# Kernel optimization log

Measured on AMD Instinct MI355X. Metric: run time of the kernel, lower is better.

## Reference

```python
import jax, jax.numpy as jnp
import numpy as np

N, F, H, C = 50000, 128, 256, 40
E = 800000
L, J = 3, 2
TOT = 7  # sum_{i<L} J**i


def setup_inputs() -> dict:
    key = jax.random.key(0)
    ks = jax.random.split(key, 16)
    def rn(k, shape, scale):
        return jax.random.normal(k, shape, jnp.float32) * scale
    w = lambda k, shape: rn(k, shape, 1.0 / np.sqrt(shape[0]).astype(np.float32))
    return {
        "x": rn(ks[0], (N, F), 1.0),
        "feature": rn(ks[1], (TOT, N, F), 1.0),
        "src": jax.random.randint(ks[2], (E,), 0, N),
        "dst": jax.random.randint(ks[3], (E,), 0, N),
        "conv_W0": w(ks[4], (F, H)),       "conv_b0": jnp.zeros((H,), jnp.float32),
        "conv_W1": w(ks[5], (2 * H, H)),   "conv_b1": jnp.zeros((H,), jnp.float32),
        "conv_W2": w(ks[6], (2 * H, H)),   "conv_b2": jnp.zeros((H,), jnp.float32),
        "lin_W0": w(ks[7], (F, H)),        "lin_b0": jnp.zeros((H,), jnp.float32),
        "lin_W1": w(ks[8], (2 * F, H)),    "lin_b1": jnp.zeros((H,), jnp.float32),
        "lin_W2": w(ks[9], (4 * F, H)),    "lin_b2": jnp.zeros((H,), jnp.float32),
        "order_weights": rn(ks[10], (J,), 1.0 / np.sqrt(J).astype(np.float32)),
        "cls_W": w(ks[11], (2 * H, C)),    "cls_b": jnp.zeros((C,), jnp.float32),
    }


def reference(x, feature, src, dst,
              conv_W0, conv_b0, conv_W1, conv_b1, conv_W2, conv_b2,
              lin_W0, lin_b0, lin_W1, lin_b1, lin_W2, lin_b2,
              order_weights, cls_W, cls_b):
    # GCN normalization with self-loops (A-hat = D^-1/2 (A+I) D^-1/2)
    loop = jnp.arange(N, dtype=src.dtype)
    src_sl = jnp.concatenate([src, loop])   # [E+N]
    dst_sl = jnp.concatenate([dst, loop])
    deg = jax.ops.segment_sum(jnp.ones_like(dst_sl, jnp.float32), dst_sl, num_segments=N)
    dinv = jax.lax.rsqrt(deg)  # deg >= 1 thanks to self loops
    norm = dinv[src_sl] * dinv[dst_sl]      # [E+N]

    def gcn(h, W, b):
        m = h @ W                            # transform first (smaller gather)
        agg = jax.ops.segment_sum(m[src_sl] * norm[:, None], dst_sl, num_segments=N)
        return agg + b

    conv_W = [conv_W0, conv_W1, conv_W2]
    conv_b = [conv_b0, conv_b1, conv_b2]
    lin_W = [lin_W0, lin_W1, lin_W2]
    lin_b = [lin_b0, lin_b1, lin_b2]

    comb = x
    begin = 0
    for i in range(L):
        convx = jax.nn.relu(gcn(comb, conv_W[i], conv_b[i]))  # [N, H]
        count = J ** i
        lf = feature[begin:begin + count]                      # [count, N, F]
        if i > 0:
            ow = jnp.tile(order_weights, J ** (i - 1)).reshape(-1, 1, 1)
            lf = ow * lf
        lf = jnp.moveaxis(lf, 0, 1).reshape(N, count * F)      # [N, count*F]
        lin_sct = jax.nn.relu(lf @ lin_W[i] + lin_b[i])        # [N, H]
        comb = jnp.concatenate([lin_sct, convx], axis=-1)      # [N, 2H]
        begin += count
    logits = gcn(comb, cls_W, cls_b)                           # [N, C]
    return jax.nn.log_softmax(logits, axis=-1), logits
```

## Files before the change

### kernel.cpp

```cpp
#include <hip/hip_runtime.h>

#define DEVI __device__ __forceinline__

namespace {

constexpr int Nn = 50000;
constexpr int Ne = 800000;
constexpr int Fd = 128;
constexpr int Hd = 256;
constexpr int Cd = 40;
constexpr int NB = (Nn + 255) / 256;

typedef __attribute__((ext_vector_type(8))) short s16x8;
typedef __attribute__((ext_vector_type(8))) unsigned short u16x8;
typedef __attribute__((ext_vector_type(4))) float f32x4;

DEVI unsigned short f2bf(float f) {
  unsigned int u = __builtin_bit_cast(unsigned int, f);
  u += 0x7fffu + ((u >> 16) & 1u);
  return (unsigned short)(u >> 16);
}
DEVI float bf2f(unsigned short s) {
  return __builtin_bit_cast(float, ((unsigned int)s) << 16);
}

DEVI void gld_lds16(const void* gptr, void* lds_base) {
  const unsigned m0v =
      (unsigned)__builtin_amdgcn_readfirstlane((unsigned)(uintptr_t)lds_base);
  asm volatile("s_mov_b32 m0, %0\n\t"
               "global_load_lds_dwordx4 %1, off"
               :: "s"(m0v), "v"(gptr) : "memory");
}

DEVI void wait_vm0_lgkm0() {
  asm volatile("s_waitcnt vmcnt(0) lgkmcnt(0)" ::: "memory");
}

DEVI void wt_one(const float* __restrict__ W, unsigned short* __restrict__ Wt,
                 int idx, int K, int H, const float* __restrict__ ow) {
  int c = idx / K, k = idx - c * K;
  int kt = k >> 6, c16 = (k >> 3) & 7, j = k & 7;
  int ksrc = (kt << 6) | ((c16 ^ (c & 7)) << 3) | j;
  float v = (c < H) ? W[(size_t)ksrc * H + c] : 0.0f;
  if (ow) v *= ow[(ksrc >> 7) & 1];
  Wt[idx] = f2bf(v);
}

constexpr int WTO0 = 0;
constexpr int WTO1 = WTO0 + 256 * 128;
constexpr int WTO2 = WTO1 + 256 * 512;
constexpr int WTO3 = WTO2 + 256 * 512;
constexpr int WTO4 = WTO3 + 256 * 128;
constexpr int WTO5 = WTO4 + 256 * 256;
constexpr int WTO6 = WTO5 + 256 * 512;
constexpr int WTO7 = WTO6 + 64 * 512;
constexpr int PREPTOT = WTO7 + Nn;

__global__ __launch_bounds__(256) void k_prep(
    const float* W0, const float* W1, const float* W2, const float* W3,
    const float* W4, const float* W5, const float* W6, const float* ow,
    unsigned short* T0, unsigned short* T1, unsigned short* T2, unsigned short* T3,
    unsigned short* T4, unsigned short* T5, unsigned short* T6, int* cnt) {
  int idx = blockIdx.x * 256 + threadIdx.x;
  if (idx >= PREPTOT) return;
  if (idx < WTO1)      wt_one(W0, T0, idx - WTO0, 128, 256, nullptr);
  else if (idx < WTO2) wt_one(W1, T1, idx - WTO1, 512, 256, nullptr);
  else if (idx < WTO3) wt_one(W2, T2, idx - WTO2, 512, 256, nullptr);
  else if (idx < WTO4) wt_one(W3, T3, idx - WTO3, 128, 256, nullptr);
  else if (idx < WTO5) wt_one(W4, T4, idx - WTO4, 256, 256, ow);
  else if (idx < WTO6) wt_one(W5, T5, idx - WTO5, 512, 256, ow);
  else if (idx < WTO7) wt_one(W6, T6, idx - WTO6, 512, 40, nullptr);
  else cnt[idx - WTO7] = 0;
}

__global__ void k_count(const int* __restrict__ dst, int* __restrict__ cnt) {
  int e = blockIdx.x * 256 + threadIdx.x;
  if (e < Ne) atomicAdd(&cnt[dst[e]], 1);
}

__global__ __launch_bounds__(256) void k_partial(const int* __restrict__ cnt,
                                                 int* __restrict__ partial) {
  __shared__ int red[256];
  const int t = threadIdx.x;
  const int i = blockIdx.x * 256 + t;
  red[t] = (i < Nn) ? cnt[i] + 1 : 0;
  __syncthreads();
#pragma unroll
  for (int off = 128; off; off >>= 1) {
    if (t < off) red[t] += red[t + off];
    __syncthreads();
  }
  if (t == 0) partial[blockIdx.x] = red[0];
}

__global__ __launch_bounds__(256) void k_scan_small(const int* __restrict__ partial,
                                                    int* __restrict__ poffs,
                                                    int* __restrict__ rowptr) {
  __shared__ int s[256];
  const int t = threadIdx.x;
  const int v = (t < NB) ? partial[t] : 0;
  s[t] = v;
  __syncthreads();
#pragma unroll
  for (int off = 1; off < 256; off <<= 1) {
    int add = (t >= off) ? s[t - off] : 0;
    __syncthreads();
    s[t] += add;
    __syncthreads();
  }
  if (t < NB) poffs[t] = s[t] - v;
  if (t == NB - 1) rowptr[Nn] = s[t];
}

__global__ __launch_bounds__(256) void k_rowptr(const int* __restrict__ cnt,
                                                const int* __restrict__ poffs,
                                                int* __restrict__ rowptr,
                                                int* __restrict__ cursor,
                                                float* __restrict__ dinv) {
  __shared__ int s[256];
  const int t = threadIdx.x;
  const int i = blockIdx.x * 256 + t;
  const int c = (i < Nn) ? cnt[i] + 1 : 0;
  s[t] = c;
  __syncthreads();
#pragma unroll
  for (int off = 1; off < 256; off <<= 1) {
    int add = (t >= off) ? s[t - off] : 0;
    __syncthreads();
    s[t] += add;
    __syncthreads();
  }
  if (i < Nn) {
    const int excl = s[t] - c + poffs[blockIdx.x];
    rowptr[i] = excl;
    cursor[i] = excl;
    dinv[i] = rsqrtf((float)c);
  }
}

__global__ void k_fill(const int* __restrict__ src, const int* __restrict__ dst,
                       const float* __restrict__ dinv, int* __restrict__ cursor,
                       int* __restrict__ csrs, float* __restrict__ csrn) {
  int e = blockIdx.x * 256 + threadIdx.x;
  if (e < Ne) {
    int s = src[e], d = dst[e];
    int pos = atomicAdd(&cursor[d], 1);
    csrs[pos] = s;
    csrn[pos] = dinv[s] * dinv[d];
  } else if (e < Ne + Nn) {
    int d = e - Ne;
    int pos = atomicAdd(&cursor[d], 1);
    csrs[pos] = d;
    float v = dinv[d];
    csrn[pos] = v * v;
  }
}

struct GRole {
  const float* A;
  const unsigned short* Wt;
  const float* bias;
  unsigned short* C;
  int K;
  int ldc;
  int relu;
};

__global__ __launch_bounds__(256) void k_gemm4(GRole R0, GRole R1, GRole R2, GRole R3) {
  const GRole R = (blockIdx.y == 0) ? R0 : (blockIdx.y == 1) ? R1
                  : (blockIdx.y == 2) ? R2 : R3;
  __shared__ char smem[49152];
  short* lA0 = (short*)smem;
  short* lA1 = (short*)(smem + 8192);
  short* lB  = (short*)(smem + 16384);
  const int tid = threadIdx.x;
  const int lane = tid & 63;
  const int wid = tid >> 6;
  const int wc = wid;
  const int row0 = blockIdx.x * 64;
  const size_t NnF = (size_t)Nn * Fd;

  f32x4 acc[4][4];
#pragma unroll
  for (int i = 0; i < 4; ++i)
#pragma unroll
    for (int j = 0; j < 4; ++j) acc[i][j] = (f32x4)0.0f;

  auto issueA = [&](int kt, f32x4 (&A4)[2][2]) {
    const int k0 = kt * 64;
    const int c = k0 >> 7;
    const int f0 = k0 & 127;
#pragma unroll
    for (int i = 0; i < 2; ++i) {
      const int v = tid * 2 + i;
      const int row = v >> 3, c16 = v & 7;
      const int grow = row0 + row;
      const bool rv = grow < Nn;
      const float* p = R.A + (size_t)c * NnF + (size_t)grow * Fd + f0 + c16 * 8;
      A4[i][0] = rv ? *(const f32x4*)p : (f32x4)0.0f;
      A4[i][1] = rv ? *(const f32x4*)(p + 4) : (f32x4)0.0f;
    }
  };
  auto writeA = [&](f32x4 (&A4)[2][2], short* lAb) {
#pragma unroll
    for (int i = 0; i < 2; ++i) {
      const int v = tid * 2 + i;
      const int row = v >> 3, c16 = v & 7;
      s16x8 val;
#pragma unroll
      for (int q = 0; q < 4; ++q) val[q] = (short)f2bf(A4[i][0][q]);
#pragma unroll
      for (int q = 0; q < 4; ++q) val[4 + q] = (short)f2bf(A4[i][1][q]);
      int byte = row * 128 + c16 * 16;
      byte ^= (row & 7) << 4;
      *(s16x8*)((char*)lAb + byte) = val;
    }
  };
  auto stageB = [&](int kt) {
    const int k0 = kt * 64;
#pragma unroll
    for (int i = 0; i < 8; ++i) {
      const int iss = wid * 8 + i;
      const int col = iss * 8 + (lane >> 3);
      gld_lds16(R.Wt + (size_t)col * R.K + k0 + (lane & 7) * 8, lB + iss * 512);
    }
  };
  auto readB = [&](s16x8 (&bv)[2][4]) {
#pragma unroll
    for (int kk = 0; kk < 2; ++kk)
#pragma unroll
      for (int ni = 0; ni < 4; ++ni) {
        int c = wc * 64 + ni * 16 + (lane & 15);
        int byte = c * 128 + kk * 64 + (lane >> 4) * 16;
        byte ^= (c & 7) << 4;
        bv[kk][ni] = *(const s16x8*)((const char*)lB + byte);
      }
  };
  auto mfma = [&](const short* lAb, s16x8 (&bv)[2][4]) {
#pragma unroll
    for (int kk = 0; kk < 2; ++kk) {
      s16x8 af[4];
#pragma unroll
      for (int mi = 0; mi < 4; ++mi) {
        int r = mi * 16 + (lane & 15);
        int byte = r * 128 + kk * 64 + (lane >> 4) * 16;
        byte ^= (r & 7) << 4;
        af[mi] = *(const s16x8*)((const char*)lAb + byte);
      }
#pragma unroll
      for (int mi = 0; mi < 4; ++mi)
#pragma unroll
        for (int ni = 0; ni < 4; ++ni)
          acc[mi][ni] = __builtin_amdgcn_mfma_f32_16x16x32_bf16(af[mi], bv[kk][ni], acc[mi][ni], 0, 0, 0);
    }
  };

  const int nkt = R.K >> 6;
  f32x4 Areg[2][2];
  issueA(0, Areg);
  stageB(0);
  writeA(Areg, lA0);
  wait_vm0_lgkm0();
  __builtin_amdgcn_s_barrier();
  for (int kt = 0; kt < nkt; ++kt) {
    short* curA = (kt & 1) ? lA1 : lA0;
    short* nxtA = (kt & 1) ? lA0 : lA1;
    s16x8 bv[2][4];
    readB(bv);
    asm volatile("s_waitcnt lgkmcnt(0)" ::: "memory");
    if (kt + 1 < nkt) { issueA(kt + 1, Areg); stageB(kt + 1); }
    mfma(curA, bv);
    if (kt + 1 < nkt) writeA(Areg, nxtA);
    wait_vm0_lgkm0();
    __builtin_amdgcn_s_barrier();
  }

  short* lC = (short*)smem;
#pragma unroll
  for (int ni = 0; ni < 4; ++ni) {
    const int col = wc * 64 + ni * 16 + (lane & 15);
    const float bvl = R.bias ? R.bias[col] : 0.0f;
#pragma unroll
    for (int mi = 0; mi < 4; ++mi) {
      const int rb = mi * 16 + ((lane >> 4) << 2);
#pragma unroll
      for (int q = 0; q < 4; ++q) {
        float vv = acc[mi][ni][q] + bvl;
        if (R.relu) vv = fmaxf(vv, 0.0f);
        lC[(rb + q) * 256 + col] = f2bf(vv);
      }
    }
  }
  __syncthreads();
#pragma unroll
  for (int p = 0; p < 8; ++p) {
    const int idx = (p * 256 + tid) * 8;
    const int row = idx >> 8;
    const int col = idx & 255;
    const int r = row0 + row;
    if (r < Nn)
      *(u16x8*)(R.C + (size_t)r * R.ldc + col) = *(const u16x8*)(lC + idx);
  }
}

__global__ __launch_bounds__(256) void k_gemmC(
    const unsigned short* __restrict__ A, int lda, int K,
    const unsigned short* __restrict__ Wt, unsigned short* __restrict__ C,
    int ldc) {
  __shared__ char smem[49152];
  short* lA0 = (short*)smem;
  short* lA1 = (short*)(smem + 8192);
  short* lB  = (short*)(smem + 16384);
  const int tid = threadIdx.x;
  const int lane = tid & 63;
  const int wid = tid >> 6;
  const int wc = wid;
  const int row0 = blockIdx.x * 64;
  const int c16a = (lane & 7) ^ ((lane >> 3) & 7);

  f32x4 acc[4][4];
#pragma unroll
  for (int i = 0; i < 4; ++i)
#pragma unroll
    for (int j = 0; j < 4; ++j) acc[i][j] = (f32x4)0.0f;

  auto stageA = [&](int kt, short* lAb) {
    const int k0 = kt * 64;
#pragma unroll
    for (int i = 0; i < 2; ++i) {
      const int iss = wid * 2 + i;
      const int row = row0 + iss * 8 + (lane >> 3);
      gld_lds16(A + (size_t)row * lda + k0 + c16a * 8, lAb + iss * 512);
    }
  };
  auto stageB = [&](int kt) {
    const int k0 = kt * 64;
#pragma unroll
    for (int i = 0; i < 8; ++i) {
      const int iss = wid * 8 + i;
      const int col = iss * 8 + (lane >> 3);
      gld_lds16(Wt + (size_t)col * K + k0 + (lane & 7) * 8, lB + iss * 512);
    }
  };
  auto readB = [&](s16x8 (&bv)[2][4]) {
#pragma unroll
    for (int kk = 0; kk < 2; ++kk)
#pragma unroll
      for (int ni = 0; ni < 4; ++ni) {
        int c = wc * 64 + ni * 16 + (lane & 15);
        int byte = c * 128 + kk * 64 + (lane >> 4) * 16;
        byte ^= (c & 7) << 4;
        bv[kk][ni] = *(const s16x8*)((const char*)lB + byte);
      }
  };
  auto mfma = [&](const short* lAb, s16x8 (&bv)[2][4]) {
#pragma unroll
    for (int kk = 0; kk < 2; ++kk) {
      s16x8 af[4];
#pragma unroll
      for (int mi = 0; mi < 4; ++mi) {
        int r = mi * 16 + (lane & 15);
        int byte = r * 128 + kk * 64 + (lane >> 4) * 16;
        byte ^= (r & 7) << 4;
        af[mi] = *(const s16x8*)((const char*)lAb + byte);
      }
#pragma unroll
      for (int mi = 0; mi < 4; ++mi)
#pragma unroll
        for (int ni = 0; ni < 4; ++ni)
          acc[mi][ni] = __builtin_amdgcn_mfma_f32_16x16x32_bf16(af[mi], bv[kk][ni], acc[mi][ni], 0, 0, 0);
    }
  };

  const int nkt = K >> 6;
  stageA(0, lA0);
  stageB(0);
  wait_vm0_lgkm0();
  __builtin_amdgcn_s_barrier();
  for (int kt = 0; kt < nkt; ++kt) {
    short* curA = (kt & 1) ? lA1 : lA0;
    short* nxtA = (kt & 1) ? lA0 : lA1;
    s16x8 bv[2][4];
    readB(bv);
    asm volatile("s_waitcnt lgkmcnt(0)" ::: "memory");
    if (kt + 1 < nkt) { stageA(kt + 1, nxtA); stageB(kt + 1); }
    mfma(curA, bv);
    wait_vm0_lgkm0();
    __builtin_amdgcn_s_barrier();
  }

  short* lC = (short*)smem;
#pragma unroll
  for (int ni = 0; ni < 4; ++ni) {
    const int col = wc * 64 + ni * 16 + (lane & 15);
#pragma unroll
    for (int mi = 0; mi < 4; ++mi) {
      const int rb = mi * 16 + ((lane >> 4) << 2);
#pragma unroll
      for (int q = 0; q < 4; ++q)
        lC[(rb + q) * 256 + col] = f2bf(acc[mi][ni][q]);
    }
  }
  __syncthreads();
#pragma unroll
  for (int p = 0; p < 8; ++p) {
    const int idx = (p * 256 + tid) * 8;
    const int row = idx >> 8;
    const int col = idx & 255;
    const int r = row0 + row;
    if (r < Nn)
      *(u16x8*)(C + (size_t)r * ldc + col) = *(const u16x8*)(lC + idx);
  }
}

__global__ __launch_bounds__(256) void k_gemmX(
    const unsigned short* __restrict__ A, int lda, int K,
    const unsigned short* __restrict__ Wt, unsigned short* __restrict__ C,
    int ldc, int ncols) {
  __shared__ char smem[81920];
  short* lAa = (short*)smem;
  short* lAbuf1 = (short*)(smem + 32768);
  short* lBa = (short*)(smem + 65536);
  short* lBbuf1 = (short*)(smem + 73728);
  const int tid = threadIdx.x;
  const int lane = tid & 63;
  const int wid = tid >> 6;
  const int wr = wid;
  const int row0 = blockIdx.x * 256;
  const int c16a = (lane & 7) ^ ((lane >> 3) & 7);

  f32x4 acc[4][4];
#pragma unroll
  for (int i = 0; i < 4; ++i)
#pragma unroll
    for (int j = 0; j < 4; ++j) acc[i][j] = (f32x4)0.0f;

  auto stage = [&](int kt, short* a, short* b) {
    const int k0 = kt * 64;
#pragma unroll
    for (int i = 0; i < 8; ++i) {
      const int iss = wid * 8 + i;
      const int row = row0 + iss * 8 + (lane >> 3);
      gld_lds16(A + (size_t)row * lda + k0 + c16a * 8, a + iss * 512);
    }
#pragma unroll
    for (int i = 0; i < 2; ++i) {
      const int iss = wid * 2 + i;
      const int col = iss * 8 + (lane >> 3);
      gld_lds16(Wt + (size_t)col * K + k0 + (lane & 7) * 8, b + iss * 512);
    }
  };
  auto compute = [&](const short* a, const short* b) {
#pragma unroll
    for (int kk = 0; kk < 2; ++kk) {
      s16x8 af[4], bv[4];
#pragma unroll
      for (int mi = 0; mi < 4; ++mi) {
        int r = wr * 64 + mi * 16 + (lane & 15);
        int byte = r * 128 + kk * 64 + (lane >> 4) * 16;
        byte ^= (r & 7) << 4;
        af[mi] = *(const s16x8*)((const char*)a + byte);
      }
#pragma unroll
      for (int ni = 0; ni < 4; ++ni) {
        int c = ni * 16 + (lane & 15);
        int byte = c * 128 + kk * 64 + (lane >> 4) * 16;
        byte ^= (c & 7) << 4;
        bv[ni] = *(const s16x8*)((const char*)b + byte);
      }
#pragma unroll
      for (int mi = 0; mi < 4; ++mi)
#pragma unroll
        for (int ni = 0; ni < 4; ++ni)
          acc[mi][ni] = __builtin_amdgcn_mfma_f32_16x16x32_bf16(af[mi], bv[ni], acc[mi][ni], 0, 0, 0);
    }
  };

  const int nkt = K >> 6;
  stage(0, lAa, lBa);
  wait_vm0_lgkm0();
  __builtin_amdgcn_s_barrier();
  for (int kt = 0; kt < nkt; ++kt) {
    short* curA = (kt & 1) ? lAbuf1 : lAa;
    short* nxtA = (kt & 1) ? lAa : lAbuf1;
    short* curB = (kt & 1) ? lBbuf1 : lBa;
    short* nxtB = (kt & 1) ? lBa : lBbuf1;
    if (kt + 1 < nkt) stage(kt + 1, nxtA, nxtB);
    compute(curA, curB);
    wait_vm0_lgkm0();
    __builtin_amdgcn_s_barrier();
  }

  short* lC = (short*)smem;
#pragma unroll
  for (int ni = 0; ni < 4; ++ni) {
    const int col = ni * 16 + (lane & 15);
#pragma unroll
    for (int mi = 0; mi < 4; ++mi) {
      const int rb = wr * 64 + mi * 16 + ((lane >> 4) << 2);
#pragma unroll
      for (int q = 0; q < 4; ++q)
        lC[(rb + q) * 64 + col] = f2bf(acc[mi][ni][q]);
    }
  }
  __syncthreads();
#pragma unroll
  for (int p = 0; p < 8; ++p) {
    const int idx = (p * 256 + tid) * 8;
    const int row = idx >> 6;
    const int col = idx & 63;
    const int r = row0 + row;
    if (r < Nn && col < ncols)
      *(u16x8*)(C + (size_t)r * ldc + col) = *(const u16x8*)(lC + idx);
  }
}

__global__ __launch_bounds__(256) void k_gather(
    const unsigned short* __restrict__ m, const int* __restrict__ rowptr,
    const int* __restrict__ csrs, const float* __restrict__ csrn,
    const float* __restrict__ bias, unsigned short* __restrict__ outp,
    int ldc, int col_off) {
  const int wid = (blockIdx.x * 256 + threadIdx.x) >> 6;
  const int lane = threadIdx.x & 63;
  if (wid >= Nn) return;
  const int half = lane >> 5;
  const int sub = lane & 31;
  const int e0 = rowptr[wid], e1 = rowptr[wid + 1];
  const unsigned short* mcol = m + sub * 8;
  float acc[8];
#pragma unroll
  for (int q = 0; q < 8; ++q) acc[q] = 0.f;

  for (int base = e0; base < e1; base += 64) {
    const int idx = base + lane;
    int s_ = 0;
    float w_ = 0.f;
    if (idx < e1) { s_ = csrs[idx]; w_ = csrn[idx]; }
    const int cn = min(64, e1 - base);
    const int npair = (cn + 1) >> 1;
    float w0, w1, w2, w3;
    u16x8 v0, v1, v2, v3;
    auto pick = [&](int p, float& w, u16x8& v) {
      if (p < npair) {
        const int j = 2 * p + half;
        const int ss = __shfl(s_, j);
        w = __shfl(w_, j);
        v = *(const u16x8*)(mcol + (size_t)ss * Hd);
      } else { w = 0.f; v = (u16x8)0; }
    };
    pick(0, w0, v0); pick(1, w1, v1); pick(2, w2, v2); pick(3, w3, v3);
    for (int p0 = 0; p0 < npair; p0 += 4) {
#pragma unroll
      for (int q = 0; q < 8; ++q) acc[q] += w0 * bf2f(v0[q]);
      pick(p0 + 4, w0, v0);
#pragma unroll
      for (int q = 0; q < 8; ++q) acc[q] += w1 * bf2f(v1[q]);
      pick(p0 + 5, w1, v1);
#pragma unroll
      for (int q = 0; q < 8; ++q) acc[q] += w2 * bf2f(v2[q]);
      pick(p0 + 6, w2, v2);
#pragma unroll
      for (int q = 0; q < 8; ++q) acc[q] += w3 * bf2f(v3[q]);
      pick(p0 + 7, w3, v3);
    }
  }

#pragma unroll
  for (int q = 0; q < 8; ++q) acc[q] += __shfl_xor(acc[q], 32);
  if (half == 0) {
    u16x8 o;
#pragma unroll
    for (int q = 0; q < 8; ++q) {
      float v = fmaxf(acc[q] + bias[sub * 8 + q], 0.f);
      o[q] = f2bf(v);
    }
    *(u16x8*)(outp + (size_t)wid * ldc + col_off + sub * 8) = o;
  }
}

__global__ __launch_bounds__(256) void k_gcls(
    const unsigned short* __restrict__ mc, const int* __restrict__ rowptr,
    const int* __restrict__ csrs, const float* __restrict__ csrn,
    const float* __restrict__ clsb, float* __restrict__ outp) {
  const int wid = (blockIdx.x * 256 + threadIdx.x) >> 6;
  const int lane = threadIdx.x & 63;
  if (wid >= Nn) return;
  const int half = lane >> 5;
  const int sub = lane & 31;
  const bool act = sub < 5;
  const int e0 = rowptr[wid], e1 = rowptr[wid + 1];
  float acc[8];
#pragma unroll
  for (int q = 0; q < 8; ++q) acc[q] = 0.f;

  for (int base = e0; base < e1; base += 64) {
    const int idx = base + lane;
    int s_ = 0;
    float w_ = 0.f;
    if (idx < e1) { s_ = csrs[idx]; w_ = csrn[idx]; }
    const int cn = min(64, e1 - base);
    const int npair = (cn + 1) >> 1;
    int sA = __shfl(s_, half);
    float wA = __shfl(w_, half);
    u16x8 vA = act ? *(const u16x8*)(mc + (size_t)sA * Cd + sub * 8) : (u16x8)0;
    for (int jj = 1; jj < npair; ++jj) {
      const int j = 2 * jj + half;
      const int sB = __shfl(s_, j);
      const float wB = __shfl(w_, j);
      const u16x8 vB = act ? *(const u16x8*)(mc + (size_t)sB * Cd + sub * 8) : (u16x8)0;
#pragma unroll
      for (int q = 0; q < 8; ++q) acc[q] += wA * bf2f(vA[q]);
      wA = wB; vA = vB;
    }
#pragma unroll
    for (int q = 0; q < 8; ++q) acc[q] += wA * bf2f(vA[q]);
  }

#pragma unroll
  for (int q = 0; q < 8; ++q) acc[q] += __shfl_xor(acc[q], 32);

  float l[8];
  float mx = -3.4e38f;
  if (act) {
#pragma unroll
    for (int q = 0; q < 8; ++q) {
      l[q] = acc[q] + clsb[sub * 8 + q];
      mx = fmaxf(mx, l[q]);
    }
  }
#pragma unroll
  for (int off = 1; off < 8; off <<= 1) mx = fmaxf(mx, __shfl_xor(mx, off));
  float se = 0.f;
  if (act) {
#pragma unroll
    for (int q = 0; q < 8; ++q) se += expf(l[q] - mx);
  }
#pragma unroll
  for (int off = 1; off < 8; off <<= 1) se += __shfl_xor(se, off);
  const float lse = mx + logf(se);
  if (half == 0 && act) {
    float* o1 = outp + (size_t)wid * Cd + sub * 8;
    float* o2 = o1 + (size_t)Nn * Cd;
#pragma unroll
    for (int q = 0; q < 8; ++q) {
      o1[q] = l[q] - lse;
      o2[q] = l[q];
    }
  }
}

}

extern "C" void kernel_launch(void* const* d_in, const int* in_sizes, int n_in,
                              void* d_out, int out_size, void* d_ws, size_t ws_size,
                              hipStream_t stream) {
  (void)in_sizes; (void)n_in; (void)out_size; (void)ws_size;
  const float* x       = (const float*)d_in[0];
  const float* feature = (const float*)d_in[1];
  const int* src       = (const int*)d_in[2];
  const int* dst       = (const int*)d_in[3];
  const float* convW[3] = {(const float*)d_in[4], (const float*)d_in[6], (const float*)d_in[8]};
  const float* convB[3] = {(const float*)d_in[5], (const float*)d_in[7], (const float*)d_in[9]};
  const float* linW[3]  = {(const float*)d_in[10], (const float*)d_in[12], (const float*)d_in[14]};
  const float* linB[3]  = {(const float*)d_in[11], (const float*)d_in[13], (const float*)d_in[15]};
  const float* oweights = (const float*)d_in[16];
  const float* clsW     = (const float*)d_in[17];
  const float* clsB     = (const float*)d_in[18];
  float* out = (float*)d_out;

  char* wsp = (char*)d_ws;
  auto alloc = [&](size_t bytes) -> void* {
    void* p = wsp;
    wsp += (bytes + 255) & ~(size_t)255;
    return p;
  };
  int* cnt      = (int*)alloc((size_t)Nn * 4);
  int* cursor   = (int*)alloc((size_t)Nn * 4);
  int* rowptr   = (int*)alloc((size_t)(Nn + 1) * 4);
  float* dinv   = (float*)alloc((size_t)Nn * 4);
  int* partial  = (int*)alloc((size_t)NB * 4);
  int* poffs    = (int*)alloc((size_t)NB * 4);
  int* csrs     = (int*)alloc((size_t)(Ne + Nn) * 4);
  float* csrn   = (float*)alloc((size_t)(Ne + Nn) * 4);
  unsigned short* WtC0 = (unsigned short*)alloc((size_t)256 * 128 * 2);
  unsigned short* WtC1 = (unsigned short*)alloc((size_t)256 * 512 * 2);
  unsigned short* WtC2 = (unsigned short*)alloc((size_t)256 * 512 * 2);
  unsigned short* WtL0 = (unsigned short*)alloc((size_t)256 * 128 * 2);
  unsigned short* WtL1 = (unsigned short*)alloc((size_t)256 * 256 * 2);
  unsigned short* WtL2 = (unsigned short*)alloc((size_t)256 * 512 * 2);
  unsigned short* WtCl = (unsigned short*)alloc((size_t)64 * 512 * 2);
  unsigned short* mbuf = (unsigned short*)alloc((size_t)Nn * Hd * 2);
  unsigned short* mcls = (unsigned short*)alloc((size_t)Nn * Cd * 2);
  unsigned short* comb0 = (unsigned short*)alloc((size_t)(Nn + 256) * 512 * 2);
  unsigned short* comb1 = (unsigned short*)alloc((size_t)(Nn + 256) * 512 * 2);
  unsigned short* comb2 = (unsigned short*)alloc((size_t)(Nn + 256) * 512 * 2);

  k_prep<<<(PREPTOT + 255) / 256, 256, 0, stream>>>(
      convW[0], convW[1], convW[2], linW[0], linW[1], linW[2], clsW, oweights,
      WtC0, WtC1, WtC2, WtL0, WtL1, WtL2, WtCl, cnt);
  k_count<<<(Ne + 255) / 256, 256, 0, stream>>>(dst, cnt);
  k_partial<<<NB, 256, 0, stream>>>(cnt, partial);
  k_scan_small<<<1, 256, 0, stream>>>(partial, poffs, rowptr);
  k_rowptr<<<NB, 256, 0, stream>>>(cnt, poffs, rowptr, cursor, dinv);
  k_fill<<<(Ne + Nn + 255) / 256, 256, 0, stream>>>(src, dst, dinv, cursor, csrs, csrn);

  const int GM = (Nn + 63) / 64;
  const int GC = (Nn + 255) / 256;
  const int GB = (Nn * 64) / 256;

  GRole rConv0{x,                              WtC0, nullptr, mbuf,  128, Hd,  0};
  GRole rLin0 {feature,                        WtL0, linB[0], comb0, 128, 512, 1};
  GRole rLin1 {feature + (size_t)1 * Nn * Fd,  WtL1, linB[1], comb1, 256, 512, 1};
  GRole rLin2 {feature + (size_t)3 * Nn * Fd,  WtL2, linB[2], comb2, 512, 512, 1};
  k_gemm4<<<dim3(GM, 4), 256, 0, stream>>>(rConv0, rLin0, rLin1, rLin2);

  k_gather<<<GB, 256, 0, stream>>>(mbuf, rowptr, csrs, csrn, convB[0], comb0, 512, 256);
  k_gemmC<<<GM, 256, 0, stream>>>(comb0, 512, 512, WtC1, mbuf, Hd);
  k_gather<<<GB, 256, 0, stream>>>(mbuf, rowptr, csrs, csrn, convB[1], comb1, 512, 256);
  k_gemmC<<<GM, 256, 0, stream>>>(comb1, 512, 512, WtC2, mbuf, Hd);
  k_gather<<<GB, 256, 0, stream>>>(mbuf, rowptr, csrs, csrn, convB[2], comb2, 512, 256);
  k_gemmX<<<GC, 256, 0, stream>>>(comb2, 512, 512, WtCl, mcls, Cd, 40);
  k_gcls<<<GB, 256, 0, stream>>>(mcls, rowptr, csrs, csrn, clsB, out);
}
```

Measured before the change: 491.4 us.

## Deepen GEMM pipelines to two-stage prefetch with partial vmcnt waits and padded epilogue

Restructures the three GEMM kernels so global-to-LDS loads for tile k+2 are issued while tile k is computed. B gets double-buffered LDS and waits use partial vmcnt counts instead of draining all outstanding loads each iteration. The bf16 epilogue staging buffer gets a padded row stride (264/72) to reduce LDS bank conflicts. Raises LDS use to 80KB per block, which may reduce occupancy, and the hand-counted vmcnt values are fragile if the instruction count changes.

```diff
diff --git a/kernel.cpp b/kernel.cpp
--- a/kernel.cpp
+++ b/kernel.cpp
@@ -30,10 +30,6 @@
   asm volatile("s_mov_b32 m0, %0\n\t"
                "global_load_lds_dwordx4 %1, off"
                :: "s"(m0v), "v"(gptr) : "memory");
-}
-
-DEVI void wait_vm0_lgkm0() {
-  asm volatile("s_waitcnt vmcnt(0) lgkmcnt(0)" ::: "memory");
 }
 
 DEVI void wt_one(const float* __restrict__ W, unsigned short* __restrict__ Wt,
@@ -169,10 +165,11 @@
 __global__ __launch_bounds__(256) void k_gemm4(GRole R0, GRole R1, GRole R2, GRole R3) {
   const GRole R = (blockIdx.y == 0) ? R0 : (blockIdx.y == 1) ? R1
                   : (blockIdx.y == 2) ? R2 : R3;
-  __shared__ char smem[49152];
+  __shared__ char smem[81920];
   short* lA0 = (short*)smem;
   short* lA1 = (short*)(smem + 8192);
-  short* lB  = (short*)(smem + 16384);
+  short* lB0 = (short*)(smem + 16384);
+  short* lB1 = (short*)(smem + 49152);
   const int tid = threadIdx.x;
   const int lane = tid & 63;
   const int wid = tid >> 6;
@@ -217,29 +214,19 @@
     }
   };
   auto stageB = [&](int kt) {
+    short* b = (kt & 1) ? lB1 : lB0;
     const int k0 = kt * 64;
 #pragma unroll
     for (int i = 0; i < 8; ++i) {
       const int iss = wid * 8 + i;
       const int col = iss * 8 + (lane >> 3);
-      gld_lds16(R.Wt + (size_t)col * R.K + k0 + (lane & 7) * 8, lB + iss * 512);
-    }
-  };
-  auto readB = [&](s16x8 (&bv)[2][4]) {
-#pragma unroll
-    for (int kk = 0; kk < 2; ++kk)
-#pragma unroll
-      for (int ni = 0; ni < 4; ++ni) {
-        int c = wc * 64 + ni * 16 + (lane & 15);
-        int byte = c * 128 + kk * 64 + (lane >> 4) * 16;
-        byte ^= (c & 7) << 4;
-        bv[kk][ni] = *(const s16x8*)((const char*)lB + byte);
-      }
-  };
-  auto mfma = [&](const short* lAb, s16x8 (&bv)[2][4]) {
+      gld_lds16(R.Wt + (size_t)col * R.K + k0 + (lane & 7) * 8, b + iss * 512);
+    }
+  };
+  auto mfma = [&](const short* lAb, const short* lBb) {
 #pragma unroll
     for (int kk = 0; kk < 2; ++kk) {
-      s16x8 af[4];
+      s16x8 af[4], bv[4];
 #pragma unroll
       for (int mi = 0; mi < 4; ++mi) {
         int r = mi * 16 + (lane & 15);
@@ -248,31 +235,41 @@
         af[mi] = *(const s16x8*)((const char*)lAb + byte);
       }
 #pragma unroll
+      for (int ni = 0; ni < 4; ++ni) {
+        int c = wc * 64 + ni * 16 + (lane & 15);
+        int byte = c * 128 + kk * 64 + (lane >> 4) * 16;
+        byte ^= (c & 7) << 4;
+        bv[ni] = *(const s16x8*)((const char*)lBb + byte);
+      }
+#pragma unroll
       for (int mi = 0; mi < 4; ++mi)
 #pragma unroll
         for (int ni = 0; ni < 4; ++ni)
-          acc[mi][ni] = __builtin_amdgcn_mfma_f32_16x16x32_bf16(af[mi], bv[kk][ni], acc[mi][ni], 0, 0, 0);
+          acc[mi][ni] = __builtin_amdgcn_mfma_f32_16x16x32_bf16(af[mi], bv[ni], acc[mi][ni], 0, 0, 0);
     }
   };
 
   const int nkt = R.K >> 6;
-  f32x4 Areg[2][2];
-  issueA(0, Areg);
+  f32x4 Ar0[2][2], Ar1[2][2];
+  issueA(0, Ar0);
   stageB(0);
-  writeA(Areg, lA0);
-  wait_vm0_lgkm0();
-  __builtin_amdgcn_s_barrier();
+  issueA(1, Ar1);
+  stageB(1);
   for (int kt = 0; kt < nkt; ++kt) {
     short* curA = (kt & 1) ? lA1 : lA0;
-    short* nxtA = (kt & 1) ? lA0 : lA1;
-    s16x8 bv[2][4];
-    readB(bv);
+    short* curB = (kt & 1) ? lB1 : lB0;
+    if (kt & 1) writeA(Ar1, curA); else writeA(Ar0, curA);
+    if (kt + 2 < nkt) {
+      if (kt & 1) issueA(kt + 2, Ar1); else issueA(kt + 2, Ar0);
+    }
+    if (kt + 2 < nkt)      asm volatile("s_waitcnt vmcnt(16)" ::: "memory");
+    else if (kt + 1 < nkt) asm volatile("s_waitcnt vmcnt(12)" ::: "memory");
+    else                   asm volatile("s_waitcnt vmcnt(0)" ::: "memory");
     asm volatile("s_waitcnt lgkmcnt(0)" ::: "memory");
-    if (kt + 1 < nkt) { issueA(kt + 1, Areg); stageB(kt + 1); }
-    mfma(curA, bv);
-    if (kt + 1 < nkt) writeA(Areg, nxtA);
-    wait_vm0_lgkm0();
     __builtin_amdgcn_s_barrier();
+    mfma(curA, curB);
+    __builtin_amdgcn_s_barrier();
+    if (kt + 2 < nkt) stageB(kt + 2);
   }
 
   short* lC = (short*)smem;
@@ -287,19 +284,20 @@
       for (int q = 0; q < 4; ++q) {
         float vv = acc[mi][ni][q] + bvl;
         if (R.relu) vv = fmaxf(vv, 0.0f);
-        lC[(rb + q) * 256 + col] = f2bf(vv);
+        lC[(rb + q) * 264 + col] = f2bf(vv);
       }
     }
   }
   __syncthreads();
 #pragma unroll
   for (int p = 0; p < 8; ++p) {
-    const int idx = (p * 256 + tid) * 8;
-    const int row = idx >> 8;
-    const int col = idx & 255;
+    const int flat = p * 256 + tid;
+    const int row = flat >> 5;
+    const int ch = flat & 31;
     const int r = row0 + row;
     if (r < Nn)
-      *(u16x8*)(R.C + (size_t)r * R.ldc + col) = *(const u16x8*)(lC + idx);
+      *(u16x8*)(R.C + (size_t)r * R.ldc + ch * 8) =
+          *(const u16x8*)(lC + row * 264 + ch * 8);
   }
 }
 
@@ -307,10 +305,11 @@
     const unsigned short* __restrict__ A, int lda, int K,
     const unsigned short* __restrict__ Wt, unsigned short* __restrict__ C,
     int ldc) {
-  __shared__ char smem[49152];
+  __shared__ char smem[81920];
   short* lA0 = (short*)smem;
   short* lA1 = (short*)(smem + 8192);
-  short* lB  = (short*)(smem + 16384);
+  short* lB0 = (short*)(smem + 16384);
+  short* lB1 = (short*)(smem + 49152);
   const int tid = threadIdx.x;
   const int lane = tid & 63;
   const int wid = tid >> 6;
@@ -324,39 +323,27 @@
 #pragma unroll
     for (int j = 0; j < 4; ++j) acc[i][j] = (f32x4)0.0f;
 
-  auto stageA = [&](int kt, short* lAb) {
+  auto stage = [&](int kt) {
+    short* a = (kt & 1) ? lA1 : lA0;
+    short* b = (kt & 1) ? lB1 : lB0;
     const int k0 = kt * 64;
 #pragma unroll
     for (int i = 0; i < 2; ++i) {
       const int iss = wid * 2 + i;
       const int row = row0 + iss * 8 + (lane >> 3);
-      gld_lds16(A + (size_t)row * lda + k0 + c16a * 8, lAb + iss * 512);
-    }
-  };
-  auto stageB = [&](int kt) {
-    const int k0 = kt * 64;
+      gld_lds16(A + (size_t)row * lda + k0 + c16a * 8, a + iss * 512);
+    }
 #pragma unroll
     for (int i = 0; i < 8; ++i) {
       const int iss = wid * 8 + i;
       const int col = iss * 8 + (lane >> 3);
-      gld_lds16(Wt + (size_t)col * K + k0 + (lane & 7) * 8, lB + iss * 512);
-    }
-  };
-  auto readB = [&](s16x8 (&bv)[2][4]) {
-#pragma unroll
-    for (int kk = 0; kk < 2; ++kk)
-#pragma unroll
-      for (int ni = 0; ni < 4; ++ni) {
-        int c = wc * 64 + ni * 16 + (lane & 15);
-        int byte = c * 128 + kk * 64 + (lane >> 4) * 16;
-        byte ^= (c & 7) << 4;
-        bv[kk][ni] = *(const s16x8*)((const char*)lB + byte);
-      }
-  };
-  auto mfma = [&](const short* lAb, s16x8 (&bv)[2][4]) {
+      gld_lds16(Wt + (size_t)col * K + k0 + (lane & 7) * 8, b + iss * 512);
+    }
+  };
+  auto mfma = [&](const short* lAb, const short* lBb) {
 #pragma unroll
     for (int kk = 0; kk < 2; ++kk) {
-      s16x8 af[4];
+      s16x8 af[4], bv[4];
 #pragma unroll
       for (int mi = 0; mi < 4; ++mi) {
         int r = mi * 16 + (lane & 15);
@@ -365,28 +352,32 @@
         af[mi] = *(const s16x8*)((const char*)lAb + byte);
       }
 #pragma unroll
+      for (int ni = 0; ni < 4; ++ni) {
+        int c = wc * 64 + ni * 16 + (lane & 15);
+        int byte = c * 128 + kk * 64 + (lane >> 4) * 16;
+        byte ^= (c & 7) << 4;
+        bv[ni] = *(const s16x8*)((const char*)lBb + byte);
+      }
+#pragma unroll
       for (int mi = 0; mi < 4; ++mi)
 #pragma unroll
         for (int ni = 0; ni < 4; ++ni)
-          acc[mi][ni] = __builtin_amdgcn_mfma_f32_16x16x32_bf16(af[mi], bv[kk][ni], acc[mi][ni], 0, 0, 0);
+          acc[mi][ni] = __builtin_amdgcn_mfma_f32_16x16x32_bf16(af[mi], bv[ni], acc[mi][ni], 0, 0, 0);
     }
   };
 
   const int nkt = K >> 6;
-  stageA(0, lA0);
-  stageB(0);
-  wait_vm0_lgkm0();
-  __builtin_amdgcn_s_barrier();
+  stage(0);
+  stage(1);
   for (int kt = 0; kt < nkt; ++kt) {
     short* curA = (kt & 1) ? lA1 : lA0;
-    short* nxtA = (kt & 1) ? lA0 : lA1;
-    s16x8 bv[2][4];
-    readB(bv);
-    asm volatile("s_waitcnt lgkmcnt(0)" ::: "memory");
-    if (kt + 1 < nkt) { stageA(kt + 1, nxtA); stageB(kt + 1); }
-    mfma(curA, bv);
-    wait_vm0_lgkm0();
+    short* curB = (kt & 1) ? lB1 : lB0;
+    if (kt + 1 < nkt) asm volatile("s_waitcnt vmcnt(10)" ::: "memory");
+    else              asm volatile("s_waitcnt vmcnt(0)" ::: "memory");
     __builtin_amdgcn_s_barrier();
+    mfma(curA, curB);
+    __builtin_amdgcn_s_barrier();
+    if (kt + 2 < nkt) stage(kt + 2);
   }
 
   short* lC = (short*)smem;
@@ -398,18 +389,19 @@
       const int rb = mi * 16 + ((lane >> 4) << 2);
 #pragma unroll
       for (int q = 0; q < 4; ++q)
-        lC[(rb + q) * 256 + col] = f2bf(acc[mi][ni][q]);
+        lC[(rb + q) * 264 + col] = f2bf(acc[mi][ni][q]);
     }
   }
   __syncthreads();
 #pragma unroll
   for (int p = 0; p < 8; ++p) {
-    const int idx = (p * 256 + tid) * 8;
-    const int row = idx >> 8;
-    const int col = idx & 255;
+    const int flat = p * 256 + tid;
+    const int row = flat >> 5;
+    const int ch = flat & 31;
     const int r = row0 + row;
     if (r < Nn)
-      *(u16x8*)(C + (size_t)r * ldc + col) = *(const u16x8*)(lC + idx);
+      *(u16x8*)(C + (size_t)r * ldc + ch * 8) =
+          *(const u16x8*)(lC + row * 264 + ch * 8);
   }
 }
 
@@ -418,10 +410,10 @@
     const unsigned short* __restrict__ Wt, unsigned short* __restrict__ C,
     int ldc, int ncols) {
   __shared__ char smem[81920];
-  short* lAa = (short*)smem;
-  short* lAbuf1 = (short*)(smem + 32768);
-  short* lBa = (short*)(smem + 65536);
-  short* lBbuf1 = (short*)(smem + 73728);
+  short* lA0 = (short*)smem;
+  short* lA1 = (short*)(smem + 32768);
+  short* lB0 = (short*)(smem + 65536);
+  short* lB1 = (short*)(smem + 73728);
   const int tid = threadIdx.x;
   const int lane = tid & 63;
   const int wid = tid >> 6;
@@ -435,7 +427,9 @@
 #pragma unroll
     for (int j = 0; j < 4; ++j) acc[i][j] = (f32x4)0.0f;
 
-  auto stage = [&](int kt, short* a, short* b) {
+  auto stage = [&](int kt) {
+    short* a = (kt & 1) ? lA1 : lA0;
+    short* b = (kt & 1) ? lB1 : lB0;
     const int k0 = kt * 64;
 #pragma unroll
     for (int i = 0; i < 8; ++i) {
@@ -450,7 +444,7 @@
       gld_lds16(Wt + (size_t)col * K + k0 + (lane & 7) * 8, b + iss * 512);
     }
   };
-  auto compute = [&](const short* a, const short* b) {
+  auto mfma = [&](const short* a, const short* b) {
 #pragma unroll
     for (int kk = 0; kk < 2; ++kk) {
       s16x8 af[4], bv[4];
@@ -477,18 +471,17 @@
   };
 
   const int nkt = K >> 6;
-  stage(0, lAa, lBa);
-  wait_vm0_lgkm0();
-  __builtin_amdgcn_s_barrier();
+  stage(0);
+  stage(1);
   for (int kt = 0; kt < nkt; ++kt) {
-    short* curA = (kt & 1) ? lAbuf1 : lAa;
-    short* nxtA = (kt & 1) ? lAa : lAbuf1;
-    short* curB = (kt & 1) ? lBbuf1 : lBa;
-    short* nxtB = (kt & 1) ? lBa : lBbuf1;
-    if (kt + 1 < nkt) stage(kt + 1, nxtA, nxtB);
-    compute(curA, curB);
-    wait_vm0_lgkm0();
+    short* curA = (kt & 1) ? lA1 : lA0;
+    short* curB = (kt & 1) ? lB1 : lB0;
+    if (kt + 1 < nkt) asm volatile("s_waitcnt vmcnt(10)" ::: "memory");
+    else              asm volatile("s_waitcnt vmcnt(0)" ::: "memory");
     __builtin_amdgcn_s_barrier();
+    mfma(curA, curB);
+    __builtin_amdgcn_s_barrier();
+    if (kt + 2 < nkt) stage(kt + 2);
   }
 
   short* lC = (short*)smem;
@@ -500,18 +493,19 @@
       const int rb = wr * 64 + mi * 16 + ((lane >> 4) << 2);
 #pragma unroll
       for (int q = 0; q < 4; ++q)
-        lC[(rb + q) * 64 + col] = f2bf(acc[mi][ni][q]);
+        lC[(rb + q) * 72 + col] = f2bf(acc[mi][ni][q]);
     }
   }
   __syncthreads();
 #pragma unroll
   for (int p = 0; p < 8; ++p) {
-    const int idx = (p * 256 + tid) * 8;
-    const int row = idx >> 6;
-    const int col = idx & 63;
+    const int flat = p * 256 + tid;
+    const int row = flat >> 3;
+    const int ch = flat & 7;
     const int r = row0 + row;
+    const int col = ch * 8;
     if (r < Nn && col < ncols)
-      *(u16x8*)(C + (size_t)r * ldc + col) = *(const u16x8*)(lC + idx);
+      *(u16x8*)(C + (size_t)r * ldc + col) = *(const u16x8*)(lC + row * 72 + col);
   }
 }
 
```

Result: faster. 480.6 us (-2.2%).
